# Optimization experiments

Measured on AMD Instinct MI355X. Metric: run time of the kernel, lower is better.

The kernel has to match this reference:

```python
import jax, jax.numpy as jnp
import numpy as np

EPS_R = 1e-6


def setup_inputs() -> dict:
    key = jax.random.key(0)
    k1, k2, k3 = jax.random.split(key, 3)
    N, F, C = 32768, 2048, 64
    X = jax.random.normal(k1, (N, F), dtype=jnp.float32)
    W = jax.random.normal(k2, (C, F), dtype=jnp.float32) * 0.1  # matches init std=0.1
    r = jax.random.uniform(k3, (F,), dtype=jnp.float32)
    return {"X": X, "W": W, "r": r}


def reference(X, W, r):
    # Weighted squared distances: d[n, c] = sum_f r_f * (X[n,f] - W[c,f])**2
    # Expanded form avoids the [N, C, F] intermediate:
    #   d = (X^2) @ r + (W^2) @ r - 2 * X @ (r * W)^T
    rc = jnp.clip(r, EPS_R, None)
    x_sq = (X * X) @ rc                      # [N]
    w_sq = (W * W) @ rc                      # [C]
    cross = X @ (W * rc).T                   # [N, C]  (dominant GEMM)
    dists = x_sq[:, None] + w_sq[None, :] - 2.0 * cross  # [N, C]
    # One prototype per class with label = class index, per init_prototypes.
    preds = jnp.argmin(dists, axis=1)        # [N] int
    return dists, preds
```

## Files before the change

### kernel.cpp

```cpp
#include <hip/hip_runtime.h>

#define NROWS 32768
#define FDIM  2048
#define CDIM  64
#define BM    64
#define BK    32
#define NCH   (FDIM / BK)
#define SA    40
#define EPS_R 1e-6f
#define WSCALE 1024.0f
#define DESCALE (2.0f / WSCALE)

typedef __attribute__((ext_vector_type(8))) _Float16 half8;
typedef __attribute__((ext_vector_type(4))) float    f32x4;

__device__ __forceinline__ unsigned packh(_Float16 a, _Float16 b) {
    return (unsigned)__builtin_bit_cast(unsigned short, a) |
           ((unsigned)__builtin_bit_cast(unsigned short, b) << 16);
}

__device__ __forceinline__ void split2(float a, float b, unsigned& hi, unsigned& lo) {
    _Float16 ha = (_Float16)a, hb = (_Float16)b;
    _Float16 la = (_Float16)(a - (float)ha), lb = (_Float16)(b - (float)hb);
    hi = packh(ha, hb);
    lo = packh(la, lb);
}

__global__ __launch_bounds__(256) void gmlvq_prep(
    const float* __restrict__ W, const float* __restrict__ r,
    unsigned short* __restrict__ Bh, unsigned short* __restrict__ Bl,
    float* __restrict__ wsq, float* __restrict__ rc_out) {
    const int c = blockIdx.x;
    const int tid = threadIdx.x;
    const int f0 = tid * 8;

    const float* Wp = W + (size_t)c * FDIM + f0;
    float4 w0 = *(const float4*)Wp;
    float4 w1 = *(const float4*)(Wp + 4);
    float4 r0 = *(const float4*)(r + f0);
    float4 r1 = *(const float4*)(r + f0 + 4);
    r0.x = fmaxf(r0.x, EPS_R); r0.y = fmaxf(r0.y, EPS_R);
    r0.z = fmaxf(r0.z, EPS_R); r0.w = fmaxf(r0.w, EPS_R);
    r1.x = fmaxf(r1.x, EPS_R); r1.y = fmaxf(r1.y, EPS_R);
    r1.z = fmaxf(r1.z, EPS_R); r1.w = fmaxf(r1.w, EPS_R);

    if (c == 0) {
        *(float4*)(rc_out + f0) = r0;
        *(float4*)(rc_out + f0 + 4) = r1;
    }

    float rw0 = r0.x * w0.x, rw1 = r0.y * w0.y, rw2 = r0.z * w0.z, rw3 = r0.w * w0.w;
    float rw4 = r1.x * w1.x, rw5 = r1.y * w1.y, rw6 = r1.z * w1.z, rw7 = r1.w * w1.w;

    float part = rw0 * w0.x + rw1 * w0.y + rw2 * w0.z + rw3 * w0.w
               + rw4 * w1.x + rw5 * w1.y + rw6 * w1.z + rw7 * w1.w;

    unsigned h01, l01, h23, l23, h45, l45, h67, l67;
    split2(rw0 * WSCALE, rw1 * WSCALE, h01, l01);
    split2(rw2 * WSCALE, rw3 * WSCALE, h23, l23);
    split2(rw4 * WSCALE, rw5 * WSCALE, h45, l45);
    split2(rw6 * WSCALE, rw7 * WSCALE, h67, l67);

    *(uint4*)(Bh + (size_t)c * FDIM + f0) = make_uint4(h01, h23, h45, h67);
    *(uint4*)(Bl + (size_t)c * FDIM + f0) = make_uint4(l01, l23, l45, l67);

#pragma unroll
    for (int m = 32; m; m >>= 1) part += __shfl_xor(part, m);
    __shared__ float red[4];
    if ((tid & 63) == 0) red[tid >> 6] = part;
    __syncthreads();
    if (tid == 0) wsq[c] = (red[0] + red[1]) + (red[2] + red[3]);
}

__global__ __launch_bounds__(256, 3) void gmlvq_main(
    const float* __restrict__ X, const float* __restrict__ rc,
    const unsigned short* __restrict__ Bh, const unsigned short* __restrict__ Bl,
    const float* __restrict__ wsq_g,
    float* __restrict__ dists, float* __restrict__ preds) {

    __shared__ __align__(16) unsigned short lds_bh[2][CDIM * SA];
    __shared__ __align__(16) unsigned short lds_bl[2][CDIM * SA];
    __shared__ float lds_xsq[BM];
    __shared__ float lds_wsq[CDIM];

    const int tid  = threadIdx.x;
    const int wave = tid >> 6;
    const int lane = tid & 63;
    const int quad = lane >> 4;
    const int l15  = lane & 15;
    const int row_base = blockIdx.x * BM;
    const int cB   = tid >> 2;
    const int segB = (tid & 3) * 8;

    if (tid < CDIM) lds_wsq[tid] = wsq_g[tid];

    const float* Ap = X + (size_t)(row_base + wave * 16 + l15) * FDIM + quad * 8;
    const float* Rp = rc + quad * 8;
    const unsigned short* Bhp = Bh + (size_t)cB * FDIM + segB;
    const unsigned short* Blp = Bl + (size_t)cB * FDIM + segB;

    uint4 b0h = *(const uint4*)(Bhp);
    uint4 b0l = *(const uint4*)(Blp);
    *(uint4*)&lds_bh[0][cB * SA + segB] = b0h;
    *(uint4*)&lds_bl[0][cB * SA + segB] = b0l;
    uint4 bnh = *(const uint4*)(Bhp + BK);
    uint4 bnl = *(const uint4*)(Blp + BK);

    float4 a0 = *(const float4*)(Ap);
    float4 a1 = *(const float4*)(Ap + 4);
    float4 r0 = *(const float4*)(Rp);
    float4 r1 = *(const float4*)(Rp + 4);

    float p = 0.f;
    f32x4 acc[4];
#pragma unroll
    for (int n = 0; n < 4; n++) acc[n] = (f32x4){0.f, 0.f, 0.f, 0.f};

#pragma unroll 2
    for (int c = 0; c < NCH; c++) {
        __syncthreads();

        const int kn = ((c + 1) & (NCH - 1)) * BK;
        const int kf = ((c + 2) & (NCH - 1)) * BK;
        const float4 a0n = *(const float4*)(Ap + kn);
        const float4 a1n = *(const float4*)(Ap + kn + 4);
        const float4 r0n = *(const float4*)(Rp + kn);
        const float4 r1n = *(const float4*)(Rp + kn + 4);
        const uint4  bfh = *(const uint4*)(Bhp + kf);
        const uint4  bfl = *(const uint4*)(Blp + kf);

        half8 ah, al;
        {
            const float va[8] = {a0.x, a0.y, a0.z, a0.w, a1.x, a1.y, a1.z, a1.w};
            const float vr[8] = {r0.x, r0.y, r0.z, r0.w, r1.x, r1.y, r1.z, r1.w};
#pragma unroll
            for (int j = 0; j < 8; j++) {
                const float v = va[j];
                const _Float16 h = (_Float16)v;
                ah[j] = h;
                al[j] = (_Float16)(v - (float)h);
                p += vr[j] * v * v;
            }
        }

        const int bb = c & 1;
#pragma unroll
        for (int n = 0; n < 4; n++) {
            const half8 bhf = *(const half8*)&lds_bh[bb][(n * 16 + l15) * SA + quad * 8];
            const half8 blf = *(const half8*)&lds_bl[bb][(n * 16 + l15) * SA + quad * 8];
            acc[n] = __builtin_amdgcn_mfma_f32_16x16x32_f16(ah, bhf, acc[n], 0, 0, 0);
            acc[n] = __builtin_amdgcn_mfma_f32_16x16x32_f16(ah, blf, acc[n], 0, 0, 0);
            acc[n] = __builtin_amdgcn_mfma_f32_16x16x32_f16(al, bhf, acc[n], 0, 0, 0);
        }

        *(uint4*)&lds_bh[bb ^ 1][cB * SA + segB] = bnh;
        *(uint4*)&lds_bl[bb ^ 1][cB * SA + segB] = bnl;

        bnh = bfh; bnl = bfl;
        a0 = a0n; a1 = a1n; r0 = r0n; r1 = r1n;
    }

    p += __shfl_xor(p, 16);
    p += __shfl_xor(p, 32);
    if (quad == 0) lds_xsq[wave * 16 + l15] = p;
    __syncthreads();

    float dd[4][4];
#pragma unroll
    for (int n = 0; n < 4; n++) {
#pragma unroll
        for (int rr = 0; rr < 4; rr++) {
            const int m = wave * 16 + quad * 4 + rr;
            const int cc = n * 16 + l15;
            const float d = lds_xsq[m] + lds_wsq[cc] - acc[n][rr] * DESCALE;
            dd[n][rr] = d;
            dists[(size_t)(row_base + m) * CDIM + cc] = d;
        }
    }

#pragma unroll
    for (int rr = 0; rr < 4; rr++) {
        float bv = dd[0][rr];
        int   bi = l15;
#pragma unroll
        for (int n = 1; n < 4; n++) {
            const float v = dd[n][rr];
            const int  ci = n * 16 + l15;
            if (v < bv || (v == bv && ci < bi)) { bv = v; bi = ci; }
        }
#pragma unroll
        for (int mask = 1; mask < 16; mask <<= 1) {
            const float ov = __shfl_xor(bv, mask);
            const int   oi = __shfl_xor(bi, mask);
            if (ov < bv || (ov == bv && oi < bi)) { bv = ov; bi = oi; }
        }
        if (l15 == 0) {
            const int m = wave * 16 + quad * 4 + rr;
            preds[row_base + m] = (float)bi;
        }
    }
}

extern "C" void kernel_launch(void* const* d_in, const int* in_sizes, int n_in,
                              void* d_out, int out_size, void* d_ws, size_t ws_size,
                              hipStream_t stream) {
    const float* X = (const float*)d_in[0];
    const float* W = (const float*)d_in[1];
    const float* r = (const float*)d_in[2];
    float* dists = (float*)d_out;
    float* preds = dists + (size_t)NROWS * CDIM;

    unsigned short* Bh = (unsigned short*)d_ws;
    unsigned short* Bl = Bh + (size_t)CDIM * FDIM;
    float* wsq   = (float*)(Bl + (size_t)CDIM * FDIM);
    float* rc_ws = wsq + CDIM;

    gmlvq_prep<<<dim3(CDIM), dim3(256), 0, stream>>>(W, r, Bh, Bl, wsq, rc_ws);
    gmlvq_main<<<dim3(NROWS / BM), dim3(256), 0, stream>>>(X, rc_ws, Bh, Bl, wsq, dists, preds);
}
```

Baseline: 388.2 us.

## Stage pre-swizzled W chunks into LDS via async global_load_lds with BK=64

The prep kernel now writes the split-fp16 W operand in a per-chunk, XOR-swizzled layout, so the main kernel can copy each 16KB chunk straight into LDS with global_load_lds. This replaces the register round-trip and padded LDS stores. The K chunk is doubled to 64, which halves the number of barriers, and the occupancy hint drops from 3 to 2 blocks per CU. The risks are no explicit wait on the async LDS loads beyond __syncthreads, larger LDS use, and lower occupancy while the kernel streams X from memory.

```diff
diff --git a/kernel.cpp b/kernel.cpp
--- a/kernel.cpp
+++ b/kernel.cpp
@@ -4,9 +4,9 @@
 #define FDIM  2048
 #define CDIM  64
 #define BM    64
-#define BK    32
+#define BK    64
 #define NCH   (FDIM / BK)
-#define SA    40
+#define CHB   16384
 #define EPS_R 1e-6f
 #define WSCALE 1024.0f
 #define DESCALE (2.0f / WSCALE)
@@ -26,9 +26,30 @@
     lo = packh(la, lb);
 }
 
+__device__ __forceinline__ void async16(const void* g, void* l) {
+    __builtin_amdgcn_global_load_lds(
+        (const __attribute__((address_space(1))) void*)g,
+        (__attribute__((address_space(3))) void*)l, 16, 0, 0);
+}
+
+__device__ __forceinline__ void split8(const float4& X0, const float4& X1,
+                                       const float4& R0, const float4& R1,
+                                       half8& AH, half8& AL, float& p) {
+    const float v_[8] = {X0.x, X0.y, X0.z, X0.w, X1.x, X1.y, X1.z, X1.w};
+    const float w_[8] = {R0.x, R0.y, R0.z, R0.w, R1.x, R1.y, R1.z, R1.w};
+#pragma unroll
+    for (int j = 0; j < 8; j++) {
+        const float v = v_[j];
+        const _Float16 h = (_Float16)v;
+        AH[j] = h;
+        AL[j] = (_Float16)(v - (float)h);
+        p += w_[j] * v * v;
+    }
+}
+
 __global__ __launch_bounds__(256) void gmlvq_prep(
     const float* __restrict__ W, const float* __restrict__ r,
-    unsigned short* __restrict__ Bh, unsigned short* __restrict__ Bl,
+    unsigned char* __restrict__ Bsw,
     float* __restrict__ wsq, float* __restrict__ rc_out) {
     const int c = blockIdx.x;
     const int tid = threadIdx.x;
@@ -61,8 +82,12 @@
     split2(rw4 * WSCALE, rw5 * WSCALE, h45, l45);
     split2(rw6 * WSCALE, rw7 * WSCALE, h67, l67);
 
-    *(uint4*)(Bh + (size_t)c * FDIM + f0) = make_uint4(h01, h23, h45, h67);
-    *(uint4*)(Bl + (size_t)c * FDIM + f0) = make_uint4(l01, l23, l45, l67);
+    const int ch = f0 >> 6;
+    const int k6 = f0 & 63;
+    const int rowoff = (k6 * 2) ^ ((c & 7) << 4);
+    unsigned char* dst = Bsw + (size_t)ch * CHB + c * 128 + rowoff;
+    *(uint4*)dst = make_uint4(h01, h23, h45, h67);
+    *(uint4*)(dst + 8192) = make_uint4(l01, l23, l45, l67);
 
 #pragma unroll
     for (int m = 32; m; m >>= 1) part += __shfl_xor(part, m);
@@ -72,14 +97,13 @@
     if (tid == 0) wsq[c] = (red[0] + red[1]) + (red[2] + red[3]);
 }
 
-__global__ __launch_bounds__(256, 3) void gmlvq_main(
+__global__ __launch_bounds__(256, 2) void gmlvq_main(
     const float* __restrict__ X, const float* __restrict__ rc,
-    const unsigned short* __restrict__ Bh, const unsigned short* __restrict__ Bl,
+    const unsigned char* __restrict__ Bsw,
     const float* __restrict__ wsq_g,
     float* __restrict__ dists, float* __restrict__ preds) {
 
-    __shared__ __align__(16) unsigned short lds_bh[2][CDIM * SA];
-    __shared__ __align__(16) unsigned short lds_bl[2][CDIM * SA];
+    __shared__ __align__(16) unsigned char lds_b[2][CHB];
     __shared__ float lds_xsq[BM];
     __shared__ float lds_wsq[CDIM];
 
@@ -89,27 +113,29 @@
     const int quad = lane >> 4;
     const int l15  = lane & 15;
     const int row_base = blockIdx.x * BM;
-    const int cB   = tid >> 2;
-    const int segB = (tid & 3) * 8;
+    const int wu = __builtin_amdgcn_readfirstlane(wave);
 
     if (tid < CDIM) lds_wsq[tid] = wsq_g[tid];
 
     const float* Ap = X + (size_t)(row_base + wave * 16 + l15) * FDIM + quad * 8;
     const float* Rp = rc + quad * 8;
-    const unsigned short* Bhp = Bh + (size_t)cB * FDIM + segB;
-    const unsigned short* Blp = Bl + (size_t)cB * FDIM + segB;
-
-    uint4 b0h = *(const uint4*)(Bhp);
-    uint4 b0l = *(const uint4*)(Blp);
-    *(uint4*)&lds_bh[0][cB * SA + segB] = b0h;
-    *(uint4*)&lds_bl[0][cB * SA + segB] = b0l;
-    uint4 bnh = *(const uint4*)(Bhp + BK);
-    uint4 bnl = *(const uint4*)(Blp + BK);
-
-    float4 a0 = *(const float4*)(Ap);
-    float4 a1 = *(const float4*)(Ap + 4);
+
+    const int col0 = ((quad ^ (l15 & 7)) << 4);
+
+    {
+        const unsigned char* src = Bsw + (size_t)wu * 4096 + lane * 16;
+        unsigned char* dst = &lds_b[0][wu * 4096];
+#pragma unroll
+        for (int j = 0; j < 4; j++) async16(src + j * 1024, dst + j * 1024);
+    }
+    float4 x0 = *(const float4*)(Ap);
+    float4 x1 = *(const float4*)(Ap + 4);
+    float4 x2 = *(const float4*)(Ap + 32);
+    float4 x3 = *(const float4*)(Ap + 36);
     float4 r0 = *(const float4*)(Rp);
     float4 r1 = *(const float4*)(Rp + 4);
+    float4 r2 = *(const float4*)(Rp + 32);
+    float4 r3 = *(const float4*)(Rp + 36);
 
     float p = 0.f;
     f32x4 acc[4];
@@ -119,45 +145,48 @@
 #pragma unroll 2
     for (int c = 0; c < NCH; c++) {
         __syncthreads();
-
-        const int kn = ((c + 1) & (NCH - 1)) * BK;
-        const int kf = ((c + 2) & (NCH - 1)) * BK;
-        const float4 a0n = *(const float4*)(Ap + kn);
-        const float4 a1n = *(const float4*)(Ap + kn + 4);
-        const float4 r0n = *(const float4*)(Rp + kn);
-        const float4 r1n = *(const float4*)(Rp + kn + 4);
-        const uint4  bfh = *(const uint4*)(Bhp + kf);
-        const uint4  bfl = *(const uint4*)(Blp + kf);
-
-        half8 ah, al;
+        const int bb = c & 1;
+        const int cn = (c + 1) & (NCH - 1);
+
         {
-            const float va[8] = {a0.x, a0.y, a0.z, a0.w, a1.x, a1.y, a1.z, a1.w};
-            const float vr[8] = {r0.x, r0.y, r0.z, r0.w, r1.x, r1.y, r1.z, r1.w};
-#pragma unroll
-            for (int j = 0; j < 8; j++) {
-                const float v = va[j];
-                const _Float16 h = (_Float16)v;
-                ah[j] = h;
-                al[j] = (_Float16)(v - (float)h);
-                p += vr[j] * v * v;
-            }
-        }
-
-        const int bb = c & 1;
+            const unsigned char* src = Bsw + (size_t)cn * CHB + wu * 4096 + lane * 16;
+            unsigned char* dst = &lds_b[bb ^ 1][wu * 4096];
+#pragma unroll
+            for (int j = 0; j < 4; j++) async16(src + j * 1024, dst + j * 1024);
+        }
+
+        const int kn = cn * BK;
+        const float4 xn0 = *(const float4*)(Ap + kn);
+        const float4 xn1 = *(const float4*)(Ap + kn + 4);
+        const float4 xn2 = *(const float4*)(Ap + kn + 32);
+        const float4 xn3 = *(const float4*)(Ap + kn + 36);
+        const float4 rn0 = *(const float4*)(Rp + kn);
+        const float4 rn1 = *(const float4*)(Rp + kn + 4);
+        const float4 rn2 = *(const float4*)(Rp + kn + 32);
+        const float4 rn3 = *(const float4*)(Rp + kn + 36);
+
+        half8 ah0, al0, ah1, al1;
+        split8(x0, x1, r0, r1, ah0, al0, p);
+        split8(x2, x3, r2, r3, ah1, al1, p);
+
+        const unsigned char* Lb = lds_b[bb];
 #pragma unroll
         for (int n = 0; n < 4; n++) {
-            const half8 bhf = *(const half8*)&lds_bh[bb][(n * 16 + l15) * SA + quad * 8];
-            const half8 blf = *(const half8*)&lds_bl[bb][(n * 16 + l15) * SA + quad * 8];
-            acc[n] = __builtin_amdgcn_mfma_f32_16x16x32_f16(ah, bhf, acc[n], 0, 0, 0);
-            acc[n] = __builtin_amdgcn_mfma_f32_16x16x32_f16(ah, blf, acc[n], 0, 0, 0);
-            acc[n] = __builtin_amdgcn_mfma_f32_16x16x32_f16(al, bhf, acc[n], 0, 0, 0);
-        }
-
-        *(uint4*)&lds_bh[bb ^ 1][cB * SA + segB] = bnh;
-        *(uint4*)&lds_bl[bb ^ 1][cB * SA + segB] = bnl;
-
-        bnh = bfh; bnl = bfl;
-        a0 = a0n; a1 = a1n; r0 = r0n; r1 = r1n;
+            const int o = ((n * 16 + l15) << 7) + col0;
+            const half8 bh0 = *(const half8*)(Lb + o);
+            const half8 bh1 = *(const half8*)(Lb + (o ^ 64));
+            const half8 bl0 = *(const half8*)(Lb + 8192 + o);
+            const half8 bl1 = *(const half8*)(Lb + 8192 + (o ^ 64));
+            acc[n] = __builtin_amdgcn_mfma_f32_16x16x32_f16(ah0, bh0, acc[n], 0, 0, 0);
+            acc[n] = __builtin_amdgcn_mfma_f32_16x16x32_f16(ah0, bl0, acc[n], 0, 0, 0);
+            acc[n] = __builtin_amdgcn_mfma_f32_16x16x32_f16(al0, bh0, acc[n], 0, 0, 0);
+            acc[n] = __builtin_amdgcn_mfma_f32_16x16x32_f16(ah1, bh1, acc[n], 0, 0, 0);
+            acc[n] = __builtin_amdgcn_mfma_f32_16x16x32_f16(ah1, bl1, acc[n], 0, 0, 0);
+            acc[n] = __builtin_amdgcn_mfma_f32_16x16x32_f16(al1, bh1, acc[n], 0, 0, 0);
+        }
+
+        x0 = xn0; x1 = xn1; x2 = xn2; x3 = xn3;
+        r0 = rn0; r1 = rn1; r2 = rn2; r3 = rn3;
     }
 
     p += __shfl_xor(p, 16);
@@ -210,11 +239,10 @@
     float* dists = (float*)d_out;
     float* preds = dists + (size_t)NROWS * CDIM;
 
-    unsigned short* Bh = (unsigned short*)d_ws;
-    unsigned short* Bl = Bh + (size_t)CDIM * FDIM;
-    float* wsq   = (float*)(Bl + (size_t)CDIM * FDIM);
+    unsigned char* Bsw = (unsigned char*)d_ws;
+    float* wsq   = (float*)(Bsw + (size_t)NCH * CHB);
     float* rc_ws = wsq + CDIM;
 
-    gmlvq_prep<<<dim3(CDIM), dim3(256), 0, stream>>>(W, r, Bh, Bl, wsq, rc_ws);
-    gmlvq_main<<<dim3(NROWS / BM), dim3(256), 0, stream>>>(X, rc_ws, Bh, Bl, wsq, dists, preds);
-}
+    gmlvq_prep<<<dim3(CDIM), dim3(256), 0, stream>>>(W, r, Bsw, wsq, rc_ws);
+    gmlvq_main<<<dim3(NROWS / BM), dim3(256), 0, stream>>>(X, rc_ws, Bsw, wsq, dists, preds);
+}
```

Measured after the change: 384.7 us. About the same (-0.9%).
